# Kernel optimization log

Hardware: AMD Instinct MI355X
Metric: run time of the kernel (lower is better)

Reference implementation:

```python
import jax, jax.numpy as jnp
import numpy as np

B, S, D, H, FF = 1, 2048, 2048, 32, 8192
HD = D // H
SCALING = HD ** -0.5
WBITS, ABITS = 8, 8
NEG = jnp.finfo(jnp.float32).min


def ste_round(x):
    # straight-through estimator round
    return x + jax.lax.stop_gradient(jnp.round(x) - x)


def fake_quant(x, bits, axis):
    # min-max asymmetric fake quantization (OmniQuant-style dynamic quant)
    qmax = float(2 ** bits - 1)
    xmin = jnp.minimum(jnp.min(x, axis=axis, keepdims=True), 0.0)
    xmax = jnp.maximum(jnp.max(x, axis=axis, keepdims=True), 0.0)
    scale = jnp.maximum((xmax - xmin) / qmax, 1e-5)
    zp = jnp.round(-xmin / scale)
    q = jnp.clip(ste_round(x / scale) + zp, 0.0, qmax)
    return (q - zp) * scale


def qlinear(x, W, b):
    # QuantLinear: quantize activation per-token, weight per-output-channel
    xq = fake_quant(x, ABITS, -1)
    Wq = fake_quant(W, WBITS, 1)  # W: [out, in], per-row (output channel)
    return xq @ Wq.T + b


def layernorm(x, g, b):
    mu = jnp.mean(x, axis=-1, keepdims=True)
    var = jnp.var(x, axis=-1, keepdims=True)
    return (x - mu) * jax.lax.rsqrt(var + 1e-5) * g + b


def setup_inputs():
    key = jax.random.key(0)
    ks = jax.random.split(key, 16)
    w = lambda k, shape: (jax.random.normal(k, shape) * 0.02).astype(jnp.float32)
    hidden_states = jax.random.normal(ks[0], (B, S, D), dtype=jnp.float32)
    causal = jnp.tril(jnp.ones((S, S), dtype=bool))
    attention_mask = jnp.where(causal, 0.0, NEG)[None, None].astype(jnp.float32)
    attention_mask = jnp.broadcast_to(attention_mask, (B, 1, S, S))
    return {
        'hidden_states': hidden_states,
        'attention_mask': attention_mask,
        'Wq': w(ks[1], (D, D)), 'bq': jnp.zeros((D,), jnp.float32),
        'Wk': w(ks[2], (D, D)), 'bk': jnp.zeros((D,), jnp.float32),
        'Wv': w(ks[3], (D, D)), 'bv': jnp.zeros((D,), jnp.float32),
        'Wo': w(ks[4], (D, D)), 'bo': jnp.zeros((D,), jnp.float32),
        'ln1_g': jnp.ones((D,), jnp.float32), 'ln1_b': jnp.zeros((D,), jnp.float32),
        'W1': w(ks[5], (FF, D)), 'b1': jnp.zeros((FF,), jnp.float32),
        'W2': w(ks[6], (D, FF)), 'b2': jnp.zeros((D,), jnp.float32),
        'ln2_g': jnp.ones((D,), jnp.float32), 'ln2_b': jnp.zeros((D,), jnp.float32),
    }


def _split_heads(x):
    # [B,S,D] -> [B,H,S,HD]
    return x.reshape(B, S, H, HD).transpose(0, 2, 1, 3)


def _layer(hidden_states, attention_mask, Wq, bq, Wk, bk, Wv, bv, Wo, bo,
           ln1_g, ln1_b, W1, b1, W2, b2, ln2_g, ln2_b):
    # ---- self attention block (do_layer_norm_before=True) ----
    residual = hidden_states
    x = layernorm(hidden_states, ln1_g, ln1_b)

    q = qlinear(x, Wq, bq) * SCALING
    q = fake_quant(q, ABITS, -1)          # qkt_matmul.quant_x1
    k = qlinear(x, Wk, bk)
    k = fake_quant(k, ABITS, -1)          # qkt_matmul.quant_x2
    v = qlinear(x, Wv, bv)
    v = fake_quant(v, ABITS, -1)          # pv_matmul.quant_x2

    qh, kh, vh = _split_heads(q), _split_heads(k), _split_heads(v)
    scores = jnp.einsum('bhqd,bhkd->bhqk', qh, kh)  # [B,H,S,S]
    scores = scores + attention_mask
    scores = jnp.maximum(scores, NEG)
    probs = jax.nn.softmax(scores, axis=-1)
    probs = fake_quant(probs, ABITS, -1)  # pv_matmul.quant_x1
    ctx = jnp.einsum('bhqk,bhkd->bhqd', probs, vh)
    ctx = ctx.transpose(0, 2, 1, 3).reshape(B, S, D)
    attn_out = qlinear(ctx, Wo, bo)
    hidden_states = residual + attn_out

    # ---- FFN block ----
    residual = hidden_states
    x = layernorm(hidden_states, ln2_g, ln2_b)
    x = jax.nn.relu(qlinear(x, W1, b1))
    x = qlinear(x, W2, b2)
    return residual + x


def reference(hidden_states, attention_mask, Wq, bq, Wk, bk, Wv, bv, Wo, bo,
              ln1_g, ln1_b, W1, b1, W2, b2, ln2_g, ln2_b):
    return _layer(hidden_states, attention_mask, Wq, bq, Wk, bk, Wv, bv, Wo, bo,
                  ln1_g, ln1_b, W1, b1, W2, b2, ln2_g, ln2_b)
```

## Files before the change

### kernel.cpp

```cpp
#include <hip/hip_runtime.h>
#include <hip/hip_bf16.h>
#include <math.h>

#define S_LEN 2048
#define D_DIM 2048
#define H_NUM 32
#define HD_DIM 64
#define FF_DIM 8192
#define QMAX 255.0f

typedef __attribute__((ext_vector_type(4))) float f32x4;
typedef __attribute__((ext_vector_type(4))) int i32x4;
typedef __attribute__((ext_vector_type(8))) __bf16 bf16x8;
typedef unsigned short u16;
typedef signed char i8;

__device__ __forceinline__ u16 f32i_to_bf16(float v) {
  return (u16)(__float_as_uint(v) >> 16);
}
__device__ __forceinline__ u16 f32_to_bf16_rne(float v) {
  __bf16 b = (__bf16)v;
  return *(u16*)&b;
}
__device__ __forceinline__ float bf16_to_f32(u16 u) {
// ... 1 lines not shown
}
__device__ __forceinline__ int pack4_i8(float q0, float q1, float q2, float q3) {
  int c0 = (int)q0 - 128, c1 = (int)q1 - 128, c2 = (int)q2 - 128, c3 = (int)q3 - 128;
  return (c0 & 0xFF) | ((c1 & 0xFF) << 8) | ((c2 & 0xFF) << 16) | ((c3 & 0xFF) << 24);
}

__device__ __forceinline__ float wred_sum(float v) {
#pragma unroll
  for (int o = 1; o < 64; o <<= 1) v += __shfl_xor(v, o, 64);
  return v;
}
__device__ __forceinline__ float wred_min(float v) {
#pragma unroll
  for (int o = 1; o < 64; o <<= 1) v = fminf(v, __shfl_xor(v, o, 64));
  return v;
}
__device__ __forceinline__ float wred_max(float v) {
#pragma unroll
  for (int o = 1; o < 64; o <<= 1) v = fmaxf(v, __shfl_xor(v, o, 64));
  return v;
}

__device__ __forceinline__ void gload_lds16(const void* g, void* l) {
  __builtin_amdgcn_global_load_lds(
      (__attribute__((address_space(1))) void*)(g),
      (__attribute__((address_space(3))) void*)(l), 16, 0, 0);
}

__device__ __forceinline__ void xcd_swz(int& bx, int& by) {
  const int gx = gridDim.x;
  const int nwg = gx * gridDim.y;
  const int orig = blockIdx.x + gx * blockIdx.y;
  const int swz = (orig & 7) * (nwg >> 3) + (orig >> 3);
  bx = swz % gx;
  by = swz / gx;
}

__global__ __launch_bounds__(256) void ln_quant_i8(const float* __restrict__ x,
                                                   const float* __restrict__ g,
                                                   const float* __restrict__ bvec,
                                                   i8* __restrict__ out,
                                                   float* __restrict__ srow,
                                                   float* __restrict__ zrow,
                                                   float* __restrict__ S0row,
                                                   float* __restrict__ S1row) {
  __shared__ float red[8];
  const int row = blockIdx.x, tid = threadIdx.x;
  const float4* xr = (const float4*)(x + (size_t)row * D_DIM);
  const float4* g4 = (const float4*)g;
  const float4* b4 = (const float4*)bvec;

  float4 v0 = xr[tid], v1 = xr[tid + 256];
  float s = v0.x + v0.y + v0.z + v0.w + v1.x + v1.y + v1.z + v1.w;
  float ss = v0.x * v0.x + v0.y * v0.y + v0.z * v0.z + v0.w * v0.w +
             v1.x * v1.x + v1.y * v1.y + v1.z * v1.z + v1.w * v1.w;
  s = wred_sum(s); ss = wred_sum(ss);
  if ((tid & 63) == 0) { red[tid >> 6] = s; red[4 + (tid >> 6)] = ss; }
  __syncthreads();
  float mu = (red[0] + red[1] + red[2] + red[3]) / (float)D_DIM;
  float var = (red[4] + red[5] + red[6] + red[7]) / (float)D_DIM - mu * mu;
  float rstd = 1.0f / sqrtf(var + 1e-5f);
  __syncthreads();

  float mn = 0.f, mx = 0.f;
  float4 n0, n1;
  {
    float4 gg = g4[tid], bb = b4[tid];
    n0.x = (v0.x - mu) * rstd * gg.x + bb.x; n0.y = (v0.y - mu) * rstd * gg.y + bb.y;
    n0.z = (v0.z - mu) * rstd * gg.z + bb.z; n0.w = (v0.w - mu) * rstd * gg.w + bb.w;
    gg = g4[tid + 256]; bb = b4[tid + 256];
    n1.x = (v1.x - mu) * rstd * gg.x + bb.x; n1.y = (v1.y - mu) * rstd * gg.y + bb.y;
    n1.z = (v1.z - mu) * rstd * gg.z + bb.z; n1.w = (v1.w - mu) * rstd * gg.w + bb.w;
    mn = fminf(mn, fminf(fminf(n0.x, n0.y), fminf(n0.z, n0.w)));
    mn = fminf(mn, fminf(fminf(n1.x, n1.y), fminf(n1.z, n1.w)));
    mx = fmaxf(mx, fmaxf(fmaxf(n0.x, n0.y), fmaxf(n0.z, n0.w)));
    mx = fmaxf(mx, fmaxf(fmaxf(n1.x, n1.y), fmaxf(n1.z, n1.w)));
  }
  mn = wred_min(mn); mx = wred_max(mx);
  if ((tid & 63) == 0) { red[tid >> 6] = mn; red[4 + (tid >> 6)] = mx; }
  __syncthreads();
  mn = fminf(fminf(red[0], red[1]), fminf(red[2], red[3]));
  mx = fmaxf(fmaxf(red[4], red[5]), fmaxf(red[6], red[7]));
  float scale = fmaxf((mx - mn) / QMAX, 1e-5f);
  float zp = rintf(-mn / scale);
  if (tid == 0) { srow[row] = scale; zrow[row] = 128.0f - zp; }

  float q00 = fminf(fmaxf(rintf(n0.x / scale) + zp, 0.f), QMAX);
  float q01 = fminf(fmaxf(rintf(n0.y / scale) + zp, 0.f), QMAX);
  float q02 = fminf(fmaxf(rintf(n0.z / scale) + zp, 0.f), QMAX);
  float q03 = fminf(fmaxf(rintf(n0.w / scale) + zp, 0.f), QMAX);
  float q10 = fminf(fmaxf(rintf(n1.x / scale) + zp, 0.f), QMAX);
  float q11 = fminf(fmaxf(rintf(n1.y / scale) + zp, 0.f), QMAX);
  float q12 = fminf(fmaxf(rintf(n1.z / scale) + zp, 0.f), QMAX);
  float q13 = fminf(fmaxf(rintf(n1.w / scale) + zp, 0.f), QMAX);
  *(int*)&out[(size_t)row * D_DIM + tid * 4] = pack4_i8(q00, q01, q02, q03);
  *(int*)&out[(size_t)row * D_DIM + 1024 + tid * 4] = pack4_i8(q10, q11, q12, q13);
  float s0 = q00 + q01 + q02 + q03 - 512.f;
  float s1 = q10 + q11 + q12 + q13 - 512.f;
  __syncthreads();
  s0 = wred_sum(s0); s1 = wred_sum(s1);
  if ((tid & 63) == 0) { red[tid >> 6] = s0; red[4 + (tid >> 6)] = s1; }
  __syncthreads();
  if (tid == 0) {
    S0row[row] = red[0] + red[1] + red[2] + red[3];
    S1row[row] = red[4] + red[5] + red[6] + red[7];
  }
}

__global__ __launch_bounds__(256) void act_quant_i8(const float* __restrict__ x,
                                                    i8* __restrict__ out,
                                                    float* __restrict__ srow,
                                                    float* __restrict__ zrow,
                                                    float* __restrict__ S0row,
                                                    float* __restrict__ S1row) {
  __shared__ float red[8];
  const int row = blockIdx.x, tid = threadIdx.x;
  const float4* xr = (const float4*)(x + (size_t)row * D_DIM);
  float4 n0 = xr[tid], n1 = xr[tid + 256];
  float mn = 0.f, mx = 0.f;
  mn = fminf(mn, fminf(fminf(n0.x, n0.y), fminf(n0.z, n0.w)));
  mn = fminf(mn, fminf(fminf(n1.x, n1.y), fminf(n1.z, n1.w)));
  mx = fmaxf(mx, fmaxf(fmaxf(n0.x, n0.y), fmaxf(n0.z, n0.w)));
  mx = fmaxf(mx, fmaxf(fmaxf(n1.x, n1.y), fmaxf(n1.z, n1.w)));
  mn = wred_min(mn); mx = wred_max(mx);
  if ((tid & 63) == 0) { red[tid >> 6] = mn; red[4 + (tid >> 6)] = mx; }
  __syncthreads();
  mn = fminf(fminf(red[0], red[1]), fminf(red[2], red[3]));
  mx = fmaxf(fmaxf(red[4], red[5]), fmaxf(red[6], red[7]));
  float scale = fmaxf((mx - mn) / QMAX, 1e-5f);
  float zp = rintf(-mn / scale);
  if (tid == 0) { srow[row] = scale; zrow[row] = 128.0f - zp; }
  float q00 = fminf(fmaxf(rintf(n0.x / scale) + zp, 0.f), QMAX);
  float q01 = fminf(fmaxf(rintf(n0.y / scale) + zp, 0.f), QMAX);
  float q02 = fminf(fmaxf(rintf(n0.z / scale) + zp, 0.f), QMAX);
  float q03 = fminf(fmaxf(rintf(n0.w / scale) + zp, 0.f), QMAX);
  float q10 = fminf(fmaxf(rintf(n1.x / scale) + zp, 0.f), QMAX);
  float q11 = fminf(fmaxf(rintf(n1.y / scale) + zp, 0.f), QMAX);
  float q12 = fminf(fmaxf(rintf(n1.z / scale) + zp, 0.f), QMAX);
  float q13 = fminf(fmaxf(rintf(n1.w / scale) + zp, 0.f), QMAX);
  *(int*)&out[(size_t)row * D_DIM + tid * 4] = pack4_i8(q00, q01, q02, q03);
  *(int*)&out[(size_t)row * D_DIM + 1024 + tid * 4] = pack4_i8(q10, q11, q12, q13);
  float s0 = q00 + q01 + q02 + q03 - 512.f;
  float s1 = q10 + q11 + q12 + q13 - 512.f;
  __syncthreads();
  s0 = wred_sum(s0); s1 = wred_sum(s1);
  if ((tid & 63) == 0) { red[tid >> 6] = s0; red[4 + (tid >> 6)] = s1; }
  __syncthreads();
  if (tid == 0) {
    S0row[row] = red[0] + red[1] + red[2] + red[3];
    S1row[row] = red[4] + red[5] + red[6] + red[7];
  }
}

__global__ __launch_bounds__(256) void wquant_i8(const float* __restrict__ W,
                                                 i8* __restrict__ Wi,
                                                 float* __restrict__ sc,
                                                 float* __restrict__ zc,
                                                 float* __restrict__ S0c,
                                                 float* __restrict__ S1c, int K) {
  __shared__ float red[8];
  const int row = blockIdx.x, tid = threadIdx.x;
  const float4* wr = (const float4*)(W + (size_t)row * K);
  const int K4 = K >> 2, H4 = K4 >> 1;
  float mn = 0.f, mx = 0.f;
  for (int i = tid; i < K4; i += 256) {
    float4 v = wr[i];
    mn = fminf(mn, fminf(fminf(v.x, v.y), fminf(v.z, v.w)));
    mx = fmaxf(mx, fmaxf(fmaxf(v.x, v.y), fmaxf(v.z, v.w)));
  }
  mn = wred_min(mn); mx = wred_max(mx);
  if ((tid & 63) == 0) { red[tid >> 6] = mn; red[4 + (tid >> 6)] = mx; }
  __syncthreads();
  mn = fminf(fminf(red[0], red[1]), fminf(red[2], red[3]));
  mx = fmaxf(fmaxf(red[4], red[5]), fmaxf(red[6], red[7]));
  float scale = fmaxf((mx - mn) / QMAX, 1e-5f);
  float zp = rintf(-mn / scale);
  if (tid == 0) { sc[row] = scale; zc[row] = 128.0f - zp; }
  float s0 = 0.f, s1 = 0.f;
  for (int i = tid; i < K4; i += 256) {
    float4 v = wr[i];
    float q0 = fminf(fmaxf(rintf(v.x / scale) + zp, 0.f), QMAX);
    float q1 = fminf(fmaxf(rintf(v.y / scale) + zp, 0.f), QMAX);
    float q2 = fminf(fmaxf(rintf(v.z / scale) + zp, 0.f), QMAX);
    float q3 = fminf(fmaxf(rintf(v.w / scale) + zp, 0.f), QMAX);
    *(int*)&Wi[(size_t)row * K + i * 4] = pack4_i8(q0, q1, q2, q3);
    float gs = q0 + q1 + q2 + q3 - 512.f;
    if (i < H4) s0 += gs; else s1 += gs;
  }
  __syncthreads();
  s0 = wred_sum(s0); s1 = wred_sum(s1);
  if ((tid & 63) == 0) { red[tid >> 6] = s0; red[4 + (tid >> 6)] = s1; }
  __syncthreads();
  if (tid == 0) {
    S0c[row] = red[0] + red[1] + red[2] + red[3];
    S1c[row] = red[4] + red[5] + red[6] + red[7];
  }
}

__global__ __launch_bounds__(256) void requant(const u16* __restrict__ vals,
                                               const float* __restrict__ tmn,
                                               const float* __restrict__ tmx,
                                               int NT, u16* __restrict__ out,
                                               float* __restrict__ srow,
                                               int N, int value_mode) {
  __shared__ float red[8];
  const int row = blockIdx.x, tid = threadIdx.x;
  float mn = 0.f, mx = 0.f;
  if (tid < NT) {
    mn = tmn ? tmn[(size_t)row * NT + tid] : 0.f;
    mx = tmx[(size_t)row * NT + tid];
  }
  mn = wred_min(mn); mx = wred_max(mx);
  if ((tid & 63) == 0) { red[tid >> 6] = mn; red[4 + (tid >> 6)] = mx; }
  __syncthreads();
  mn = fminf(fminf(red[0], red[1]), fminf(red[2], red[3]));
  mx = fmaxf(fmaxf(red[4], red[5]), fmaxf(red[6], red[7]));
  mn = fminf(mn, 0.f); mx = fmaxf(mx, 0.f);
  float scale = fmaxf((mx - mn) / QMAX, 1e-5f);
  float zp = rintf(-mn / scale);
  if (srow && tid == 0) srow[row] = scale;
  const ushort4* vr = (const ushort4*)(vals + (size_t)row * N);
  ushort4* orow = (ushort4*)(out + (size_t)row * N);
  const int N4 = N >> 2;
  for (int i = tid; i < N4; i += 256) {
    ushort4 u = vr[i];
    float q0 = fminf(fmaxf(rintf(bf16_to_f32(u.x) / scale) + zp, 0.f), QMAX) - zp;
    float q1 = fminf(fmaxf(rintf(bf16_to_f32(u.y) / scale) + zp, 0.f), QMAX) - zp;
    float q2 = fminf(fmaxf(rintf(bf16_to_f32(u.z) / scale) + zp, 0.f), QMAX) - zp;
    float q3 = fminf(fmaxf(rintf(bf16_to_f32(u.w) / scale) + zp, 0.f), QMAX) - zp;
    ushort4 o;
    if (value_mode) {
      o.x = f32_to_bf16_rne(q0 * scale); o.y = f32_to_bf16_rne(q1 * scale);
      o.z = f32_to_bf16_rne(q2 * scale); o.w = f32_to_bf16_rne(q3 * scale);
    } else {
      o.x = f32i_to_bf16(q0); o.y = f32i_to_bf16(q1);
      o.z = f32i_to_bf16(q2); o.w = f32i_to_bf16(q3);
    }
    orow[i] = o;
  }
}

__global__ __launch_bounds__(256) void requant_ff_i8(const u16* __restrict__ vals,
                                                     const float* __restrict__ tmx,
                                                     i8* __restrict__ out,
                                                     float* __restrict__ srow,
                                                     float* __restrict__ zrow,
                                                     float* __restrict__ S0row,
                                                     float* __restrict__ S1row) {
  __shared__ float red[8];
  const int row = blockIdx.x, tid = threadIdx.x;
  float mx = (tid < 128) ? tmx[(size_t)row * 128 + tid] : 0.f;
  mx = wred_max(mx);
  if ((tid & 63) == 0) red[tid >> 6] = mx;
  __syncthreads();
  mx = fmaxf(fmaxf(red[0], red[1]), fmaxf(red[2], red[3]));
  mx = fmaxf(mx, 0.f);
  float scale = fmaxf(mx / QMAX, 1e-5f);
  if (tid == 0) { srow[row] = scale; zrow[row] = 128.0f; }
  const ushort4* vr = (const ushort4*)(vals + (size_t)row * FF_DIM);
  const int N4 = FF_DIM >> 2;
  float s0 = 0.f, s1 = 0.f;
  for (int i = tid; i < N4; i += 256) {
    ushort4 u = vr[i];
    float q0 = fminf(fmaxf(rintf(bf16_to_f32(u.x) / scale), 0.f), QMAX);
    float q1 = fminf(fmaxf(rintf(bf16_to_f32(u.y) / scale), 0.f), QMAX);
    float q2 = fminf(fmaxf(rintf(bf16_to_f32(u.z) / scale), 0.f), QMAX);
    float q3 = fminf(fmaxf(rintf(bf16_to_f32(u.w) / scale), 0.f), QMAX);
    *(int*)&out[(size_t)row * FF_DIM + i * 4] = pack4_i8(q0, q1, q2, q3);
    float gs = q0 + q1 + q2 + q3 - 512.f;
    if (i < 1024) s0 += gs; else s1 += gs;
  }
  __syncthreads();
  s0 = wred_sum(s0); s1 = wred_sum(s1);
  if ((tid & 63) == 0) { red[tid >> 6] = s0; red[4 + (tid >> 6)] = s1; }
  __syncthreads();
  if (tid == 0) {
    S0row[row] = red[0] + red[1] + red[2] + red[3];
    S1row[row] = red[4] + red[5] + red[6] + red[7];
  }
}

__device__ __forceinline__ void gemm128_i8_db(
    const i8* __restrict__ A, const i8* __restrict__ B,
    int K, int bm, int bn, int k_begin, int k_end,
    i8* As, i8* Bs, i32x4 (&acc)[4][4]) {
  const int tid = threadIdx.x;
  const int wid = tid >> 6, lane = tid & 63;
  const int wr = wid >> 1, wc = wid & 1;
  const int lr = lane & 15, lk = lane >> 4;
  const int r0 = tid >> 2, c0 = (tid & 3) * 16;
  const int r1 = 64 + r0;
  const size_t ldsb0 = (size_t)(wid * 64) * 16;
  const size_t ldsb1 = (size_t)(256 + wid * 64) * 16;

  const i8* Ag0 = A + (size_t)(bm + r0) * K + c0;
  const i8* Ag1 = A + (size_t)(bm + r1) * K + c0;
  const i8* Bg0 = B + (size_t)(bn + r0) * K + c0;
  const i8* Bg1 = B + (size_t)(bn + r1) * K + c0;

  const int nt = (k_end - k_begin) >> 6;

#define STAGE_I8(t)                                   \
  {                                                   \
    const int _k = k_begin + (t) * 64;                \
    i8* _Ab = As + (size_t)((t) & 1) * 8192;          \
    i8* _Bb = Bs + (size_t)((t) & 1) * 8192;          \
    gload_lds16(Ag0 + _k, _Ab + ldsb0);               \
    gload_lds16(Ag1 + _k, _Ab + ldsb1);               \
    gload_lds16(Bg0 + _k, _Bb + ldsb0);               \
    gload_lds16(Bg1 + _k, _Bb + ldsb1);               \
  }

  STAGE_I8(0);
  __syncthreads();

  for (int t = 0; t < nt; ++t) {
    const i8* Ac = As + (size_t)(t & 1) * 8192;
    const i8* Bc = Bs + (size_t)(t & 1) * 8192;
    i32x4 af[4], bf[4];
#pragma unroll
    for (int mi = 0; mi < 4; ++mi)
      af[mi] = *(const i32x4*)&Ac[(size_t)(wr * 64 + mi * 16 + lr) * 64 + lk * 16];
#pragma unroll
    for (int ni = 0; ni < 4; ++ni)
      bf[ni] = *(const i32x4*)&Bc[(size_t)(wc * 64 + ni * 16 + lr) * 64 + lk * 16];
    if (t + 1 < nt) STAGE_I8(t + 1);
#pragma unroll
    for (int mi = 0; mi < 4; ++mi)
#pragma unroll
      for (int ni = 0; ni < 4; ++ni)
        acc[mi][ni] = __builtin_amdgcn_mfma_i32_16x16x64_i8(af[mi], bf[ni], acc[mi][ni], 0, 0, 0);
    __syncthreads();
  }
#undef STAGE_I8
}

__global__ __launch_bounds__(256) void gemm_qkv_i8(
    const i8* __restrict__ A, const float* __restrict__ sx, const float* __restrict__ zx,
    const float* __restrict__ Sx0, const float* __restrict__ Sx1,
    const i8* __restrict__ Bq, const float* __restrict__ sbq, const float* __restrict__ zbq,
    const float* __restrict__ Sq0, const float* __restrict__ Sq1,
    const float* __restrict__ biasq, u16* __restrict__ Cq,
    float* __restrict__ tqmn, float* __restrict__ tqmx,
    const i8* __restrict__ Bk, const float* __restrict__ sbk, const float* __restrict__ zbk,
    const float* __restrict__ Sk0, const float* __restrict__ Sk1,
    const float* __restrict__ biask, u16* __restrict__ Ck,
    float* __restrict__ tkmn, float* __restrict__ tkmx,
    const i8* __restrict__ Bv, const float* __restrict__ sbv, const float* __restrict__ zbv,
    const float* __restrict__ Sv0, const float* __restrict__ Sv1,
    const float* __restrict__ biasv, u16* __restrict__ Cv,
    float* __restrict__ tvmn, float* __restrict__ tvmx) {
  __shared__ __align__(16) i8 As[2 * 128 * 64], Bs[2 * 128 * 64];
  int bx, by; xcd_swz(bx, by);
  const int which = bx >> 4;
  const int bn = (bx & 15) * 128;
  const int bm = by * 128;
  const i8* B = (which == 0) ? Bq : (which == 1) ? Bk : Bv;
  const float* sb = (which == 0) ? sbq : (which == 1) ? sbk : sbv;
  const float* zb = (which == 0) ? zbq : (which == 1) ? zbk : zbv;
  const float* Sb0 = (which == 0) ? Sq0 : (which == 1) ? Sk0 : Sv0;
  const float* Sb1 = (which == 0) ? Sq1 : (which == 1) ? Sk1 : Sv1;
  const float* bias = (which == 0) ? biasq : (which == 1) ? biask : biasv;
  u16* C = (which == 0) ? Cq : (which == 1) ? Ck : Cv;
  float* tmn = (which == 0) ? tqmn : (which == 1) ? tkmn : tvmn;
  float* tmx = (which == 0) ? tqmx : (which == 1) ? tkmx : tvmx;
  const float alpha = (which == 0) ? 0.125f : 1.0f;

  i32x4 acc[4][4] = {};
  gemm128_i8_db(A, B, D_DIM, bm, bn, 0, D_DIM, As, Bs, acc);

  const int tid = threadIdx.x;
  const int wid = tid >> 6, lane = tid & 63;
  const int wr = wid >> 1, wc = wid & 1;
  const int lr = lane & 15, lk = lane >> 4;
  const int col0 = bn + wc * 64 + lr;
  const int rbase = bm + wr * 64 + lk * 4;
  const int tci = (bn >> 6) + wc;
// ... 84 lines not shown
      mxv = fmaxf(mxv, __shfl_xor(mxv, 2, 64));
      mxv = fmaxf(mxv, __shfl_xor(mxv, 4, 64));
      mxv = fmaxf(mxv, __shfl_xor(mxv, 8, 64));
      if (lr == 0) tmx[(size_t)row * 128 + tci] = mxv;
    }
  }
}

__global__ __launch_bounds__(256) void gemm_splitk_i8(
    const i8* __restrict__ A, const float* __restrict__ sx, const float* __restrict__ zx,
    const float* __restrict__ Sx0, const float* __restrict__ Sx1,
    const i8* __restrict__ B, const float* __restrict__ sb, const float* __restrict__ zb,
    const float* __restrict__ Sb0, const float* __restrict__ Sb1,
    float* __restrict__ part, int N, int K) {
  __shared__ __align__(16) i8 As[2 * 128 * 64], Bs[2 * 128 * 64];
  int bx, by; xcd_swz(bx, by);
  const int bm = by * 128, bn = bx * 128;
  const int ks = blockIdx.z;
  const int kchunk = K >> 1;
  i32x4 acc[4][4] = {};
  gemm128_i8_db(A, B, K, bm, bn, ks * kchunk, (ks + 1) * kchunk, As, Bs, acc);

  const float* Sxz = ks ? Sx1 : Sx0;
  const float* Sbz = ks ? Sb1 : Sb0;
  const float kcf = (float)kchunk;
  float* dst = part + (size_t)ks * S_LEN * N;
  const int tid = threadIdx.x;
  const int wid = tid >> 6, lane = tid & 63;
  const int wr = wid >> 1, wc = wid & 1;
  const int lr = lane & 15, lk = lane >> 4;
  const int col0 = bn + wc * 64 + lr;
  const int rbase = bm + wr * 64 + lk * 4;
#pragma unroll
  for (int ni = 0; ni < 4; ++ni) {
    const int col = col0 + ni * 16;
    const float sbc = sb[col], zbc = zb[col], Sbc = Sbz[col];
#pragma unroll
    for (int mi = 0; mi < 4; ++mi)
#pragma unroll
      for (int r = 0; r < 4; ++r) {
        const int row = rbase + mi * 16 + r;
        const float zar = zx[row];
        float ci = (float)acc[mi][ni][r] + zar * Sbc + zbc * Sxz[row] + kcf * zar * zbc;
        dst[(size_t)row * N + col] = sx[row] * sbc * ci;
      }
  }
}

__global__ __launch_bounds__(256) void splitk_reduce(
    const float* __restrict__ part,
    const float* __restrict__ bias, const float* __restrict__ res,
    float* __restrict__ out, int N) {
  const size_t stride4 = (size_t)S_LEN * N / 4;
  const int n4 = N >> 2;
  for (size_t i = (size_t)blockIdx.x * 256 + threadIdx.x; i < stride4;
       i += (size_t)gridDim.x * 256) {
    float4 s = ((const float4*)part)[i];
    float4 p = ((const float4*)part)[i + stride4];
    s.x += p.x; s.y += p.y; s.z += p.z; s.w += p.w;
    float4 b4 = ((const float4*)bias)[i % n4];
    s.x += b4.x; s.y += b4.y; s.z += b4.z; s.w += b4.w;
    if (res) {
      float4 r = ((const float4*)res)[i];
      s.x += r.x; s.y += r.y; s.z += r.z; s.w += r.w;
    }
    ((float4*)out)[i] = s;
  }
}

__global__ __launch_bounds__(256) void splitk_reduce_ln(
    const float* __restrict__ part,
    const float* __restrict__ bias, const float* __restrict__ res,
    float* __restrict__ h2out,
    const float* __restrict__ g, const float* __restrict__ bvec,
    i8* __restrict__ out, float* __restrict__ srow, float* __restrict__ zrow,
    float* __restrict__ S0row, float* __restrict__ S1row) {
  __shared__ float red[8];
  const int row = blockIdx.x, tid = threadIdx.x;
  const float4* p0 = (const float4*)(part + (size_t)row * D_DIM);
  const float4* p1 = (const float4*)(part + (size_t)S_LEN * D_DIM + (size_t)row * D_DIM);
  const float4* rr = (const float4*)(res + (size_t)row * D_DIM);
  const float4* b4 = (const float4*)bias;
  const float4* g4 = (const float4*)g;
  const float4* e4 = (const float4*)bvec;

  float4 a0 = p0[tid], a1 = p0[tid + 256];
  float4 q0 = p1[tid], q1 = p1[tid + 256];
  float4 r0 = rr[tid], r1 = rr[tid + 256];
  float4 c0 = b4[tid], c1 = b4[tid + 256];
  float4 v0, v1;
  v0.x = a0.x + q0.x + c0.x + r0.x; v0.y = a0.y + q0.y + c0.y + r0.y;
  v0.z = a0.z + q0.z + c0.z + r0.z; v0.w = a0.w + q0.w + c0.w + r0.w;
  v1.x = a1.x + q1.x + c1.x + r1.x; v1.y = a1.y + q1.y + c1.y + r1.y;
  v1.z = a1.z + q1.z + c1.z + r1.z; v1.w = a1.w + q1.w + c1.w + r1.w;
  float* h2r = h2out + (size_t)row * D_DIM;
  *(float4*)&h2r[tid * 4] = v0;
  *(float4*)&h2r[1024 + tid * 4] = v1;

  float s = v0.x + v0.y + v0.z + v0.w + v1.x + v1.y + v1.z + v1.w;
  float ss = v0.x * v0.x + v0.y * v0.y + v0.z * v0.z + v0.w * v0.w +
             v1.x * v1.x + v1.y * v1.y + v1.z * v1.z + v1.w * v1.w;
  s = wred_sum(s); ss = wred_sum(ss);
  if ((tid & 63) == 0) { red[tid >> 6] = s; red[4 + (tid >> 6)] = ss; }
  __syncthreads();
  float mu = (red[0] + red[1] + red[2] + red[3]) / (float)D_DIM;
  float var = (red[4] + red[5] + red[6] + red[7]) / (float)D_DIM - mu * mu;
  float rstd = 1.0f / sqrtf(var + 1e-5f);
  __syncthreads();

  float mn = 0.f, mx = 0.f;
  float4 n0, n1;
  {
    float4 gg = g4[tid], bb = e4[tid];
    n0.x = (v0.x - mu) * rstd * gg.x + bb.x; n0.y = (v0.y - mu) * rstd * gg.y + bb.y;
    n0.z = (v0.z - mu) * rstd * gg.z + bb.z; n0.w = (v0.w - mu) * rstd * gg.w + bb.w;
    gg = g4[tid + 256]; bb = e4[tid + 256];
    n1.x = (v1.x - mu) * rstd * gg.x + bb.x; n1.y = (v1.y - mu) * rstd * gg.y + bb.y;
    n1.z = (v1.z - mu) * rstd * gg.z + bb.z; n1.w = (v1.w - mu) * rstd * gg.w + bb.w;
    mn = fminf(mn, fminf(fminf(n0.x, n0.y), fminf(n0.z, n0.w)));
    mn = fminf(mn, fminf(fminf(n1.x, n1.y), fminf(n1.z, n1.w)));
    mx = fmaxf(mx, fmaxf(fmaxf(n0.x, n0.y), fmaxf(n0.z, n0.w)));
    mx = fmaxf(mx, fmaxf(fmaxf(n1.x, n1.y), fmaxf(n1.z, n1.w)));
  }
  mn = wred_min(mn); mx = wred_max(mx);
  if ((tid & 63) == 0) { red[tid >> 6] = mn; red[4 + (tid >> 6)] = mx; }
  __syncthreads();
  mn = fminf(fminf(red[0], red[1]), fminf(red[2], red[3]));
  mx = fmaxf(fmaxf(red[4], red[5]), fmaxf(red[6], red[7]));
  float scale = fmaxf((mx - mn) / QMAX, 1e-5f);
  float zp = rintf(-mn / scale);
  if (tid == 0) { srow[row] = scale; zrow[row] = 128.0f - zp; }
  float q00 = fminf(fmaxf(rintf(n0.x / scale) + zp, 0.f), QMAX);
  float q01 = fminf(fmaxf(rintf(n0.y / scale) + zp, 0.f), QMAX);
  float q02 = fminf(fmaxf(rintf(n0.z / scale) + zp, 0.f), QMAX);
  float q03 = fminf(fmaxf(rintf(n0.w / scale) + zp, 0.f), QMAX);
  float q10 = fminf(fmaxf(rintf(n1.x / scale) + zp, 0.f), QMAX);
  float q11 = fminf(fmaxf(rintf(n1.y / scale) + zp, 0.f), QMAX);
  float q12 = fminf(fmaxf(rintf(n1.z / scale) + zp, 0.f), QMAX);
  float q13 = fminf(fmaxf(rintf(n1.w / scale) + zp, 0.f), QMAX);
  *(int*)&out[(size_t)row * D_DIM + tid * 4] = pack4_i8(q00, q01, q02, q03);
  *(int*)&out[(size_t)row * D_DIM + 1024 + tid * 4] = pack4_i8(q10, q11, q12, q13);
  float s0 = q00 + q01 + q02 + q03 - 512.f;
  float s1 = q10 + q11 + q12 + q13 - 512.f;
  __syncthreads();
  s0 = wred_sum(s0); s1 = wred_sum(s1);
  if ((tid & 63) == 0) { red[tid >> 6] = s0; red[4 + (tid >> 6)] = s1; }
  __syncthreads();
  if (tid == 0) {
    S0row[row] = red[0] + red[1] + red[2] + red[3];
    S1row[row] = red[4] + red[5] + red[6] + red[7];
  }
}

__global__ __launch_bounds__(256) void attn_fused(
    const u16* __restrict__ qi, const float* __restrict__ sq,
    const u16* __restrict__ ki, const float* __restrict__ sk,
    const u16* __restrict__ vf, float* __restrict__ ctx) {
  __shared__ __align__(16) u16 Qs[64][72];
  __shared__ __align__(16) u16 Ks[64][72];
  __shared__ __align__(16) u16 Ps[64][72];
  __shared__ __align__(16) u16 Vt[64][72];
  const int bid = blockIdx.x;
  const int ti = (S_LEN / 64 - 1) - (bid >> 5);
  const int h = bid & (H_NUM - 1);
  const int i0 = ti * 64;
  const int tid = threadIdx.x;
  const int wid = tid >> 6, lane = tid & 63;
  const int lr = lane & 15, g = lane >> 4;
  const size_t hbase = (size_t)h * HD_DIM;

  const int r_a = tid >> 3, ch_a = tid & 7;
  const int r_b = 32 + r_a;
  const int jr_v = tid & 63, ch_v = tid >> 6;

  for (int c = tid; c < 512; c += 256) {
    int r = c >> 3, ch = c & 7;
    *(float4*)&Qs[r][ch * 8] =
        *(const float4*)&qi[(size_t)(i0 + r) * D_DIM + hbase + ch * 8];
  }
  float sq4[4];
#pragma unroll
  for (int r = 0; r < 4; ++r) sq4[r] = sq[i0 + wid * 16 + g * 4 + r];
  __syncthreads();

  const int ntiles = i0 / 64 + 1;
  float m_r[4] = {-1e30f, -1e30f, -1e30f, -1e30f};
  float l_r[4] = {0.f, 0.f, 0.f, 0.f};

  float4 ka0 = *(const float4*)&ki[(size_t)r_a * D_DIM + hbase + ch_a * 8];
  float4 ka1 = *(const float4*)&ki[(size_t)r_b * D_DIM + hbase + ch_a * 8];
  for (int t = 0; t < ntiles; ++t) {
    __syncthreads();
    *(float4*)&Ks[r_a][ch_a * 8] = ka0;
    *(float4*)&Ks[r_b][ch_a * 8] = ka1;
    __syncthreads();
    if (t + 1 < ntiles) {
      const int jn = (t + 1) * 64;
      ka0 = *(const float4*)&ki[(size_t)(jn + r_a) * D_DIM + hbase + ch_a * 8];
      ka1 = *(const float4*)&ki[(size_t)(jn + r_b) * D_DIM + hbase + ch_a * 8];
    }

    bf16x8 aq0 = *(const bf16x8*)&Qs[wid * 16 + lr][g * 8];
    bf16x8 aq1 = *(const bf16x8*)&Qs[wid * 16 + lr][32 + g * 8];
    f32x4 accs[4] = {};
#pragma unroll
    for (int ni = 0; ni < 4; ++ni) {
      bf16x8 b0 = *(const bf16x8*)&Ks[ni * 16 + lr][g * 8];
      bf16x8 b1 = *(const bf16x8*)&Ks[ni * 16 + lr][32 + g * 8];
      accs[ni] = __builtin_amdgcn_mfma_f32_16x16x32_bf16(aq0, b0, accs[ni], 0, 0, 0);
      accs[ni] = __builtin_amdgcn_mfma_f32_16x16x32_bf16(aq1, b1, accs[ni], 0, 0, 0);
    }

    const int jt = t * 64;
    float sv[4][4];
#pragma unroll
    for (int ni = 0; ni < 4; ++ni) {
      const float skc = sk[jt + ni * 16 + lr];
#pragma unroll
      for (int r = 0; r < 4; ++r) sv[ni][r] = accs[ni][r] * sq4[r] * skc;
    }
    if (t == ntiles - 1) {
      const int jcol = jt + lr, irow = i0 + wid * 16 + g * 4;
#pragma unroll
      for (int ni = 0; ni < 4; ++ni)
#pragma unroll
        for (int r = 0; r < 4; ++r)
          if (jcol + ni * 16 > irow + r) sv[ni][r] = -1e30f;
    }
#pragma unroll
    for (int r = 0; r < 4; ++r) {
      float tmax = fmaxf(fmaxf(sv[0][r], sv[1][r]), fmaxf(sv[2][r], sv[3][r]));
      tmax = fmaxf(tmax, __shfl_xor(tmax, 1, 64));
      tmax = fmaxf(tmax, __shfl_xor(tmax, 2, 64));
      tmax = fmaxf(tmax, __shfl_xor(tmax, 4, 64));
      tmax = fmaxf(tmax, __shfl_xor(tmax, 8, 64));
      float mnew = fmaxf(m_r[r], tmax);
      float sum = __expf(sv[0][r] - mnew) + __expf(sv[1][r] - mnew) +
                  __expf(sv[2][r] - mnew) + __expf(sv[3][r] - mnew);
      sum += __shfl_xor(sum, 1, 64);
      sum += __shfl_xor(sum, 2, 64);
      sum += __shfl_xor(sum, 4, 64);
      sum += __shfl_xor(sum, 8, 64);
      l_r[r] = l_r[r] * __expf(m_r[r] - mnew) + sum;
      m_r[r] = mnew;
    }
  }

  float qsc[4], idn[4];
#pragma unroll
  for (int r = 0; r < 4; ++r) {
    float sc = fmaxf((1.0f / l_r[r]) / QMAX, 1e-5f);
    qsc[r] = sc;
    idn[r] = 1.0f / (l_r[r] * sc);
  }

  f32x4 acco[4] = {};
  float4 kb0 = *(const float4*)&ki[(size_t)r_a * D_DIM + hbase + ch_a * 8];
  float4 kb1 = *(const float4*)&ki[(size_t)r_b * D_DIM + hbase + ch_a * 8];
  float4 vb0 = *(const float4*)&vf[(size_t)jr_v * D_DIM + hbase + ch_v * 8];
  float4 vb1 = *(const float4*)&vf[(size_t)jr_v * D_DIM + hbase + (4 + ch_v) * 8];
  for (int t = 0; t < ntiles; ++t) {
    __syncthreads();
    *(float4*)&Ks[r_a][ch_a * 8] = kb0;
    *(float4*)&Ks[r_b][ch_a * 8] = kb1;
    {
      const u16* v0 = (const u16*)&vb0;
      const u16* v1 = (const u16*)&vb1;
#pragma unroll
      for (int e = 0; e < 8; ++e) Vt[ch_v * 8 + e][jr_v] = v0[e];
#pragma unroll
      for (int e = 0; e < 8; ++e) Vt[(4 + ch_v) * 8 + e][jr_v] = v1[e];
    }
    __syncthreads();
    if (t + 1 < ntiles) {
      const int jn = (t + 1) * 64;
      kb0 = *(const float4*)&ki[(size_t)(jn + r_a) * D_DIM + hbase + ch_a * 8];
      kb1 = *(const float4*)&ki[(size_t)(jn + r_b) * D_DIM + hbase + ch_a * 8];
      vb0 = *(const float4*)&vf[(size_t)(jn + jr_v) * D_DIM + hbase + ch_v * 8];
      vb1 = *(const float4*)&vf[(size_t)(jn + jr_v) * D_DIM + hbase + (4 + ch_v) * 8];
    }

    bf16x8 aq0 = *(const bf16x8*)&Qs[wid * 16 + lr][g * 8];
    bf16x8 aq1 = *(const bf16x8*)&Qs[wid * 16 + lr][32 + g * 8];
    f32x4 accs[4] = {};
#pragma unroll
    for (int ni = 0; ni < 4; ++ni) {
      bf16x8 b0 = *(const bf16x8*)&Ks[ni * 16 + lr][g * 8];
      bf16x8 b1 = *(const bf16x8*)&Ks[ni * 16 + lr][32 + g * 8];
      accs[ni] = __builtin_amdgcn_mfma_f32_16x16x32_bf16(aq0, b0, accs[ni], 0, 0, 0);
      accs[ni] = __builtin_amdgcn_mfma_f32_16x16x32_bf16(aq1, b1, accs[ni], 0, 0, 0);
    }

    const int jt = t * 64;
    const bool diag = (t == ntiles - 1);
    const int jcol = jt + lr, irow = i0 + wid * 16 + g * 4;
#pragma unroll
    for (int ni = 0; ni < 4; ++ni) {
      const float skc = sk[jt + ni * 16 + lr];
#pragma unroll
      for (int r = 0; r < 4; ++r) {
        float s = accs[ni][r] * sq4[r] * skc;
        if (diag && (jcol + ni * 16 > irow + r)) s = -1e30f;
        float e = __expf(s - m_r[r]);
        float q8 = fminf(fmaxf(rintf(e * idn[r]), 0.f), QMAX);
        Ps[wid * 16 + g * 4 + r][ni * 16 + lr] = f32i_to_bf16(q8);
      }
    }

    bf16x8 ap0 = *(const bf16x8*)&Ps[wid * 16 + lr][g * 8];
    bf16x8 ap1 = *(const bf16x8*)&Ps[wid * 16 + lr][32 + g * 8];
#pragma unroll
    for (int ni = 0; ni < 4; ++ni) {
      bf16x8 b0 = *(const bf16x8*)&Vt[ni * 16 + lr][g * 8];
      bf16x8 b1 = *(const bf16x8*)&Vt[ni * 16 + lr][32 + g * 8];
      acco[ni] = __builtin_amdgcn_mfma_f32_16x16x32_bf16(ap0, b0, acco[ni], 0, 0, 0);
      acco[ni] = __builtin_amdgcn_mfma_f32_16x16x32_bf16(ap1, b1, acco[ni], 0, 0, 0);
    }
  }

#pragma unroll
  for (int ni = 0; ni < 4; ++ni)
#pragma unroll
    for (int r = 0; r < 4; ++r) {
      const int row = i0 + wid * 16 + g * 4 + r;
      ctx[(size_t)row * D_DIM + hbase + ni * 16 + lr] = acco[ni][r] * qsc[r];
    }
}

extern "C" void kernel_launch(void* const* d_in, const int* in_sizes, int n_in,
                              void* d_out, int out_size, void* d_ws, size_t ws_size,
                              hipStream_t stream) {
  (void)in_sizes; (void)n_in; (void)out_size;
  const float* hs  = (const float*)d_in[0];
  const float* Wq  = (const float*)d_in[2];
  const float* bq  = (const float*)d_in[3];
  const float* Wk  = (const float*)d_in[4];
  const float* bk  = (const float*)d_in[5];
  const float* Wv  = (const float*)d_in[6];
  const float* bv  = (const float*)d_in[7];
  const float* Wo  = (const float*)d_in[8];
  const float* bo  = (const float*)d_in[9];
  const float* g1  = (const float*)d_in[10];
  const float* be1 = (const float*)d_in[11];
  const float* W1  = (const float*)d_in[12];
  const float* bf1 = (const float*)d_in[13];
  const float* W2  = (const float*)d_in[14];
  const float* bf2 = (const float*)d_in[15];
  const float* g2  = (const float*)d_in[16];
  const float* be2 = (const float*)d_in[17];
  float* out = (float*)d_out;

  const size_t SD = (size_t)S_LEN * D_DIM;
  const size_t SF = (size_t)S_LEN * FF_DIM;

  char* p = (char*)d_ws;
  auto alloc = [&](size_t bytes) { char* r = p; p += (bytes + 255) & ~(size_t)255; return r; };

  float* h2   = (float*)alloc(SD * 4);
  float* sx   = (float*)alloc(S_LEN * 4);
  float* zx   = (float*)alloc(S_LEN * 4);
  float* Sx0  = (float*)alloc(S_LEN * 4);
  float* Sx1  = (float*)alloc(S_LEN * 4);
  float* sxf  = (float*)alloc(S_LEN * 4);
  float* zxf  = (float*)alloc(S_LEN * 4);
  float* Sf0  = (float*)alloc(S_LEN * 4);
  float* Sf1  = (float*)alloc(S_LEN * 4);
  float* sqv  = (float*)alloc(S_LEN * 4);
  float* skv  = (float*)alloc(S_LEN * 4);
  float* swq = (float*)alloc(D_DIM * 4); float* zwq = (float*)alloc(D_DIM * 4);
  float* Sq0 = (float*)alloc(D_DIM * 4); float* Sq1 = (float*)alloc(D_DIM * 4);
  float* swk = (float*)alloc(D_DIM * 4); float* zwk = (float*)alloc(D_DIM * 4);
  float* Sk0 = (float*)alloc(D_DIM * 4); float* Sk1 = (float*)alloc(D_DIM * 4);
  float* swv = (float*)alloc(D_DIM * 4); float* zwv = (float*)alloc(D_DIM * 4);
  float* Sv0 = (float*)alloc(D_DIM * 4); float* Sv1 = (float*)alloc(D_DIM * 4);
  float* swo = (float*)alloc(D_DIM * 4); float* zwo = (float*)alloc(D_DIM * 4);
  float* So0 = (float*)alloc(D_DIM * 4); float* So1 = (float*)alloc(D_DIM * 4);
  float* sw1 = (float*)alloc(FF_DIM * 4); float* zw1 = (float*)alloc(FF_DIM * 4);
  float* S10 = (float*)alloc(FF_DIM * 4); float* S11 = (float*)alloc(FF_DIM * 4);
  float* sw2 = (float*)alloc(D_DIM * 4); float* zw2 = (float*)alloc(D_DIM * 4);
  float* S20 = (float*)alloc(D_DIM * 4); float* S21 = (float*)alloc(D_DIM * 4);
  float* tqmn = (float*)alloc(S_LEN * 32 * 4);
  float* tqmx = (float*)alloc(S_LEN * 32 * 4);
  float* tkmn = (float*)alloc(S_LEN * 32 * 4);
  float* tkmx = (float*)alloc(S_LEN * 32 * 4);
  float* tvmn = (float*)alloc(S_LEN * 32 * 4);
  float* tvmx = (float*)alloc(S_LEN * 32 * 4);
  float* tf1x = (float*)alloc(S_LEN * 128 * 4);
  i8* xi  = (i8*)alloc(SD);
  i8* wqi = (i8*)alloc(SD);
  i8* wki = (i8*)alloc(SD);
  i8* wvi = (i8*)alloc(SD);
  i8* woi = (i8*)alloc(SD);
  i8* w1i = (i8*)alloc(SF);
  i8* w2i = (i8*)alloc(SF);
  i8* f1i = (i8*)alloc(SF);
  char* arena = alloc(8 * SD * 2);
  u16* qv   = (u16*)arena;
  u16* kv   = qv + SD;
  u16* vv   = kv + SD;
  u16* qi8  = vv + SD;
  u16* ki8  = qi8 + SD;
  u16* vfb  = ki8 + SD;
  float* ctxb = (float*)(vfb + SD);
  float* pwo = (float*)arena;
  u16* f1v = (u16*)arena;
  float* pw2 = (float*)(arena + 4 * SD * 2);
  size_t need = (size_t)(p - (char*)d_ws);
  if (ws_size < need) return;

  dim3 blk(256);

  wquant_i8<<<D_DIM, blk, 0, stream>>>(Wq, wqi, swq, zwq, Sq0, Sq1, D_DIM);
  wquant_i8<<<D_DIM, blk, 0, stream>>>(Wk, wki, swk, zwk, Sk0, Sk1, D_DIM);
  wquant_i8<<<D_DIM, blk, 0, stream>>>(Wv, wvi, swv, zwv, Sv0, Sv1, D_DIM);
  wquant_i8<<<D_DIM, blk, 0, stream>>>(Wo, woi, swo, zwo, So0, So1, D_DIM);
  wquant_i8<<<FF_DIM, blk, 0, stream>>>(W1, w1i, sw1, zw1, S10, S11, D_DIM);
  wquant_i8<<<D_DIM, blk, 0, stream>>>(W2, w2i, sw2, zw2, S20, S21, FF_DIM);

  ln_quant_i8<<<S_LEN, blk, 0, stream>>>(hs, g1, be1, xi, sx, zx, Sx0, Sx1);

  dim3 gqkv(3 * D_DIM / 128, S_LEN / 128);
  gemm_qkv_i8<<<gqkv, blk, 0, stream>>>(xi, sx, zx, Sx0, Sx1,
                                        wqi, swq, zwq, Sq0, Sq1, bq, qv, tqmn, tqmx,
                                        wki, swk, zwk, Sk0, Sk1, bk, kv, tkmn, tkmx,
                                        wvi, swv, zwv, Sv0, Sv1, bv, vv, tvmn, tvmx);

  requant<<<S_LEN, blk, 0, stream>>>(qv, tqmn, tqmx, 32, qi8, sqv, D_DIM, 0);
  requant<<<S_LEN, blk, 0, stream>>>(kv, tkmn, tkmx, 32, ki8, skv, D_DIM, 0);
  requant<<<S_LEN, blk, 0, stream>>>(vv, tvmn, tvmx, 32, vfb, nullptr, D_DIM, 1);

  attn_fused<<<(S_LEN / 64) * H_NUM, blk, 0, stream>>>(qi8, sqv, ki8, skv, vfb, ctxb);

  act_quant_i8<<<S_LEN, blk, 0, stream>>>(ctxb, xi, sx, zx, Sx0, Sx1);

  dim3 gwo(D_DIM / 128, S_LEN / 128, 2);
  gemm_splitk_i8<<<gwo, blk, 0, stream>>>(xi, sx, zx, Sx0, Sx1,
                                          woi, swo, zwo, So0, So1, pwo, D_DIM, D_DIM);
  splitk_reduce_ln<<<S_LEN, blk, 0, stream>>>(pwo, bo, hs, h2, g2, be2,
                                              xi, sx, zx, Sx0, Sx1);

  dim3 gff(FF_DIM / 128, S_LEN / 128);
  gemm_w1_i8<<<gff, blk, 0, stream>>>(xi, sx, zx, Sx0, Sx1,
                                      w1i, sw1, zw1, S10, S11, bf1, f1v, tf1x);
  requant_ff_i8<<<S_LEN, blk, 0, stream>>>(f1v, tf1x, f1i, sxf, zxf, Sf0, Sf1);

  dim3 gw2(D_DIM / 128, S_LEN / 128, 2);
  gemm_splitk_i8<<<gw2, blk, 0, stream>>>(f1i, sxf, zxf, Sf0, Sf1,
                                          w2i, sw2, zw2, S20, S21, pw2, D_DIM, FF_DIM);
  splitk_reduce<<<2048, blk, 0, stream>>>(pw2, bf2, h2, out, D_DIM);
}
```

Baseline: 470.3 us.

## Merge weight-quant and requant launches; split attention into stats and PV kernels

Folds the four DxD weight-quantization launches into one grid and the three Q/K/V requant launches into one grid, which cuts kernel-launch and tail overhead. Splits the fused attention kernel into two kernels. The first computes the per-row softmax max and sum and writes them to global buffers. The second reloads them and does the probability quantization and PV matmul. This lowers shared-memory use per kernel, which may allow higher occupancy, but the QK^T scores are now computed twice and two extra HxS buffers are written and read.

```diff
diff --git a/kernel.cpp b/kernel.cpp
--- a/kernel.cpp
+++ b/kernel.cpp
@@ -177,15 +177,16 @@
   }
 }
 
-__global__ __launch_bounds__(256) void wquant_i8(const float* __restrict__ W,
-                                                 i8* __restrict__ Wi,
-                                                 float* __restrict__ sc,
-                                                 float* __restrict__ zc,
-                                                 float* __restrict__ S0c,
-                                                 float* __restrict__ S1c, int K) {
+__device__ __forceinline__ void wquant_body(const float* __restrict__ wr0,
+                                            i8* __restrict__ wo,
+                                            float* __restrict__ sc,
+                                            float* __restrict__ zc,
+                                            float* __restrict__ S0c,
+                                            float* __restrict__ S1c,
+                                            int row, int K) {
   __shared__ float red[8];
-  const int row = blockIdx.x, tid = threadIdx.x;
-  const float4* wr = (const float4*)(W + (size_t)row * K);
+  const int tid = threadIdx.x;
+  const float4* wr = (const float4*)wr0;
   const int K4 = K >> 2, H4 = K4 >> 1;
   float mn = 0.f, mx = 0.f;
   for (int i = tid; i < K4; i += 256) {
@@ -208,7 +209,7 @@
     float q1 = fminf(fmaxf(rintf(v.y / scale) + zp, 0.f), QMAX);
     float q2 = fminf(fmaxf(rintf(v.z / scale) + zp, 0.f), QMAX);
     float q3 = fminf(fmaxf(rintf(v.w / scale) + zp, 0.f), QMAX);
-    *(int*)&Wi[(size_t)row * K + i * 4] = pack4_i8(q0, q1, q2, q3);
+    *(int*)&wo[i * 4] = pack4_i8(q0, q1, q2, q3);
     float gs = q0 + q1 + q2 + q3 - 512.f;
     if (i < H4) s0 += gs; else s1 += gs;
   }
@@ -222,18 +223,54 @@
   }
 }
 
-__global__ __launch_bounds__(256) void requant(const u16* __restrict__ vals,
-                                               const float* __restrict__ tmn,
-                                               const float* __restrict__ tmx,
-                                               int NT, u16* __restrict__ out,
-                                               float* __restrict__ srow,
-                                               int N, int value_mode) {
+__global__ __launch_bounds__(256) void wquant_i8(const float* __restrict__ W,
+                                                 i8* __restrict__ Wi,
+                                                 float* __restrict__ sc,
+                                                 float* __restrict__ zc,
+                                                 float* __restrict__ S0c,
+                                                 float* __restrict__ S1c, int K) {
+  const int row = blockIdx.x;
+  wquant_body(W + (size_t)row * K, Wi + (size_t)row * K, sc, zc, S0c, S1c, row, K);
+}
+
+__global__ __launch_bounds__(256) void wquant4_i8(
+    const float* __restrict__ W0, i8* __restrict__ O0, float* s0, float* z0, float* a0, float* b0,
+    const float* __restrict__ W1, i8* __restrict__ O1, float* s1, float* z1, float* a1, float* b1,
+    const float* __restrict__ W2, i8* __restrict__ O2, float* s2, float* z2, float* a2, float* b2,
+    const float* __restrict__ W3, i8* __restrict__ O3, float* s3, float* z3, float* a3, float* b3) {
+  const int which = blockIdx.x >> 11;
+  const int row = blockIdx.x & (D_DIM - 1);
+  const float* W = (which == 0) ? W0 : (which == 1) ? W1 : (which == 2) ? W2 : W3;
+  i8* O = (which == 0) ? O0 : (which == 1) ? O1 : (which == 2) ? O2 : O3;
+  float* sc = (which == 0) ? s0 : (which == 1) ? s1 : (which == 2) ? s2 : s3;
+  float* zc = (which == 0) ? z0 : (which == 1) ? z1 : (which == 2) ? z2 : z3;
+  float* Sa = (which == 0) ? a0 : (which == 1) ? a1 : (which == 2) ? a2 : a3;
+  float* Sb = (which == 0) ? b0 : (which == 1) ? b1 : (which == 2) ? b2 : b3;
+  wquant_body(W + (size_t)row * D_DIM, O + (size_t)row * D_DIM, sc, zc, Sa, Sb, row, D_DIM);
+}
+
+__global__ __launch_bounds__(256) void requant3(
+    const u16* __restrict__ qv, const float* __restrict__ tqmn, const float* __restrict__ tqmx,
+    u16* __restrict__ qo, float* __restrict__ sqv,
+    const u16* __restrict__ kv, const float* __restrict__ tkmn, const float* __restrict__ tkmx,
+    u16* __restrict__ ko, float* __restrict__ skv,
+    const u16* __restrict__ vv, const float* __restrict__ tvmn, const float* __restrict__ tvmx,
+    u16* __restrict__ vo) {
   __shared__ float red[8];
-  const int row = blockIdx.x, tid = threadIdx.x;
+  const int wh = blockIdx.x >> 11;
+  const int row = blockIdx.x & (S_LEN - 1);
+  const int tid = threadIdx.x;
+  const u16* vals = (wh == 0) ? qv : (wh == 1) ? kv : vv;
+  const float* tmn = (wh == 0) ? tqmn : (wh == 1) ? tkmn : tvmn;
+  const float* tmx = (wh == 0) ? tqmx : (wh == 1) ? tkmx : tvmx;
+  u16* out = (wh == 0) ? qo : (wh == 1) ? ko : vo;
+  float* srow = (wh == 0) ? sqv : (wh == 1) ? skv : nullptr;
+  const int value_mode = (wh == 2) ? 1 : 0;
+
   float mn = 0.f, mx = 0.f;
-  if (tid < NT) {
-    mn = tmn ? tmn[(size_t)row * NT + tid] : 0.f;
-    mx = tmx[(size_t)row * NT + tid];
+  if (tid < 32) {
+    mn = tmn[(size_t)row * 32 + tid];
+    mx = tmx[(size_t)row * 32 + tid];
   }
   mn = wred_min(mn); mx = wred_max(mx);
   if ((tid & 63) == 0) { red[tid >> 6] = mn; red[4 + (tid >> 6)] = mx; }
@@ -244,10 +281,9 @@
   float scale = fmaxf((mx - mn) / QMAX, 1e-5f);
   float zp = rintf(-mn / scale);
   if (srow && tid == 0) srow[row] = scale;
-  const ushort4* vr = (const ushort4*)(vals + (size_t)row * N);
-  ushort4* orow = (ushort4*)(out + (size_t)row * N);
-  const int N4 = N >> 2;
-  for (int i = tid; i < N4; i += 256) {
+  const ushort4* vr = (const ushort4*)(vals + (size_t)row * D_DIM);
+  ushort4* orow = (ushort4*)(out + (size_t)row * D_DIM);
+  for (int i = tid; i < D_DIM / 4; i += 256) {
     ushort4 u = vr[i];
     float q0 = fminf(fmaxf(rintf(bf16_to_f32(u.x) / scale) + zp, 0.f), QMAX) - zp;
     float q1 = fminf(fmaxf(rintf(bf16_to_f32(u.y) / scale) + zp, 0.f), QMAX) - zp;
@@ -638,14 +674,12 @@
   }
 }
 
-__global__ __launch_bounds__(256) void attn_fused(
+__global__ __launch_bounds__(256) void attn_ml(
     const u16* __restrict__ qi, const float* __restrict__ sq,
     const u16* __restrict__ ki, const float* __restrict__ sk,
-    const u16* __restrict__ vf, float* __restrict__ ctx) {
+    float* __restrict__ Mb, float* __restrict__ Lb) {
   __shared__ __align__(16) u16 Qs[64][72];
   __shared__ __align__(16) u16 Ks[64][72];
-  __shared__ __align__(16) u16 Ps[64][72];
-  __shared__ __align__(16) u16 Vt[64][72];
   const int bid = blockIdx.x;
   const int ti = (S_LEN / 64 - 1) - (bid >> 5);
   const int h = bid & (H_NUM - 1);
@@ -657,7 +691,6 @@
 
   const int r_a = tid >> 3, ch_a = tid & 7;
   const int r_b = 32 + r_a;
-  const int jr_v = tid & 63, ch_v = tid >> 6;
 
   for (int c = tid; c < 512; c += 256) {
     int r = c >> 3, ch = c & 7;
@@ -732,14 +765,58 @@
     }
   }
 
-  float qsc[4], idn[4];
+  if (lr == 0) {
+#pragma unroll
+    for (int r = 0; r < 4; ++r) {
+      const int row = i0 + wid * 16 + g * 4 + r;
+      Mb[(size_t)h * S_LEN + row] = m_r[r];
+      Lb[(size_t)h * S_LEN + row] = l_r[r];
+    }
+  }
+}
+
+__global__ __launch_bounds__(256) void attn_pv(
+    const u16* __restrict__ qi, const float* __restrict__ sq,
+    const u16* __restrict__ ki, const float* __restrict__ sk,
+    const u16* __restrict__ vf,
+    const float* __restrict__ Mb, const float* __restrict__ Lb,
+    float* __restrict__ ctx) {
+  __shared__ __align__(16) u16 Qs[64][72];
+  __shared__ __align__(16) u16 Ks[64][72];
+  __shared__ __align__(16) u16 Ps[64][72];
+  __shared__ __align__(16) u16 Vt[64][72];
+  const int bid = blockIdx.x;
+  const int ti = (S_LEN / 64 - 1) - (bid >> 5);
+  const int h = bid & (H_NUM - 1);
+  const int i0 = ti * 64;
+  const int tid = threadIdx.x;
+  const int wid = tid >> 6, lane = tid & 63;
+  const int lr = lane & 15, g = lane >> 4;
+  const size_t hbase = (size_t)h * HD_DIM;
+
+  const int r_a = tid >> 3, ch_a = tid & 7;
+  const int r_b = 32 + r_a;
+  const int jr_v = tid & 63, ch_v = tid >> 6;
+
+  for (int c = tid; c < 512; c += 256) {
+    int r = c >> 3, ch = c & 7;
+    *(float4*)&Qs[r][ch * 8] =
+        *(const float4*)&qi[(size_t)(i0 + r) * D_DIM + hbase + ch * 8];
+  }
+  float sq4[4], m_r[4], qsc[4], idn[4];
 #pragma unroll
   for (int r = 0; r < 4; ++r) {
-    float sc = fmaxf((1.0f / l_r[r]) / QMAX, 1e-5f);
+    const int row = i0 + wid * 16 + g * 4 + r;
+    sq4[r] = sq[row];
+    m_r[r] = Mb[(size_t)h * S_LEN + row];
+    float li = Lb[(size_t)h * S_LEN + row];
+    float sc = fmaxf((1.0f / li) / QMAX, 1e-5f);
     qsc[r] = sc;
-    idn[r] = 1.0f / (l_r[r] * sc);
-  }
-
+    idn[r] = 1.0f / (li * sc);
+  }
+  __syncthreads();
+
+  const int ntiles = i0 / 64 + 1;
   f32x4 acco[4] = {};
   float4 kb0 = *(const float4*)&ki[(size_t)r_a * D_DIM + hbase + ch_a * 8];
   float4 kb1 = *(const float4*)&ki[(size_t)r_b * D_DIM + hbase + ch_a * 8];
@@ -838,6 +915,7 @@
 
   const size_t SD = (size_t)S_LEN * D_DIM;
   const size_t SF = (size_t)S_LEN * FF_DIM;
+  const size_t HS = (size_t)H_NUM * S_LEN;
 
   char* p = (char*)d_ws;
   auto alloc = [&](size_t bytes) { char* r = p; p += (bytes + 255) & ~(size_t)255; return r; };
@@ -853,6 +931,8 @@
   float* Sf1  = (float*)alloc(S_LEN * 4);
   float* sqv  = (float*)alloc(S_LEN * 4);
   float* skv  = (float*)alloc(S_LEN * 4);
+  float* Mb   = (float*)alloc(HS * 4);
+  float* Lbv  = (float*)alloc(HS * 4);
   float* swq = (float*)alloc(D_DIM * 4); float* zwq = (float*)alloc(D_DIM * 4);
   float* Sq0 = (float*)alloc(D_DIM * 4); float* Sq1 = (float*)alloc(D_DIM * 4);
   float* swk = (float*)alloc(D_DIM * 4); float* zwk = (float*)alloc(D_DIM * 4);
@@ -896,10 +976,11 @@
 
   dim3 blk(256);
 
-  wquant_i8<<<D_DIM, blk, 0, stream>>>(Wq, wqi, swq, zwq, Sq0, Sq1, D_DIM);
-  wquant_i8<<<D_DIM, blk, 0, stream>>>(Wk, wki, swk, zwk, Sk0, Sk1, D_DIM);
-  wquant_i8<<<D_DIM, blk, 0, stream>>>(Wv, wvi, swv, zwv, Sv0, Sv1, D_DIM);
-  wquant_i8<<<D_DIM, blk, 0, stream>>>(Wo, woi, swo, zwo, So0, So1, D_DIM);
+  wquant4_i8<<<4 * D_DIM, blk, 0, stream>>>(
+      Wq, wqi, swq, zwq, Sq0, Sq1,
+      Wk, wki, swk, zwk, Sk0, Sk1,
+      Wv, wvi, swv, zwv, Sv0, Sv1,
+      Wo, woi, swo, zwo, So0, So1);
   wquant_i8<<<FF_DIM, blk, 0, stream>>>(W1, w1i, sw1, zw1, S10, S11, D_DIM);
   wquant_i8<<<D_DIM, blk, 0, stream>>>(W2, w2i, sw2, zw2, S20, S21, FF_DIM);
 
@@ -911,11 +992,13 @@
                                         wki, swk, zwk, Sk0, Sk1, bk, kv, tkmn, tkmx,
                                         wvi, swv, zwv, Sv0, Sv1, bv, vv, tvmn, tvmx);
 
-  requant<<<S_LEN, blk, 0, stream>>>(qv, tqmn, tqmx, 32, qi8, sqv, D_DIM, 0);
-  requant<<<S_LEN, blk, 0, stream>>>(kv, tkmn, tkmx, 32, ki8, skv, D_DIM, 0);
-  requant<<<S_LEN, blk, 0, stream>>>(vv, tvmn, tvmx, 32, vfb, nullptr, D_DIM, 1);
-
-  attn_fused<<<(S_LEN / 64) * H_NUM, blk, 0, stream>>>(qi8, sqv, ki8, skv, vfb, ctxb);
+  requant3<<<3 * S_LEN, blk, 0, stream>>>(qv, tqmn, tqmx, qi8, sqv,
+                                          kv, tkmn, tkmx, ki8, skv,
+                                          vv, tvmn, tvmx, vfb);
+
+  const int ga = (S_LEN / 64) * H_NUM;
+  attn_ml<<<ga, blk, 0, stream>>>(qi8, sqv, ki8, skv, Mb, Lbv);
+  attn_pv<<<ga, blk, 0, stream>>>(qi8, sqv, ki8, skv, vfb, Mb, Lbv, ctxb);
 
   act_quant_i8<<<S_LEN, blk, 0, stream>>>(ctxb, xi, sx, zx, Sx0, Sx1);
 
```

Measured after the change: 458.0 us. -2.6%, faster.
